# Performance work log

Measured on AMD Instinct MI355X. Metric: run time of the kernel, lower is better.

## Reference

```python
import jax, jax.numpy as jnp
import numpy as np

T, MEM, B, DM, N, D = 1024, 1024, 4, 1024, 16, 64
C = MEM + T
SCALE = 1.0 / D ** 0.5
LN_EPS = 1e-5


def _rel_shift(x):
    # x: [T, C, B, N] -> Transformer-XL relative shift
    t, c = x.shape[0], x.shape[1]
    zero_pad = jnp.zeros((t, 1) + x.shape[2:], x.dtype)
    x_padded = jnp.concatenate([zero_pad, x], axis=1)  # [T, C+1, B, N]
    x_padded = x_padded.reshape((c + 1, t) + x.shape[2:])
    return x_padded[1:].reshape(x.shape)


def setup_inputs() -> dict:
    key = jax.random.key(0)
    ks = jax.random.split(key, 8)
    h = jax.random.normal(ks[0], (T, B, DM), jnp.float32)
    m = jax.random.normal(ks[1], (MEM, B, DM), jnp.float32)
    r = jax.random.normal(ks[2], (C, DM), jnp.float32)
    # causal mask with memory: query i (global pos MEM+i) may attend to j <= MEM+i
    mask = (jnp.arange(C)[None, :] > (jnp.arange(T)[:, None] + MEM))[:, :, None]  # [T,C,1] bool, True=disallow
    W_qkv = jax.random.normal(ks[3], (DM, 3 * N * D), jnp.float32) * 0.02
    W_r = jax.random.normal(ks[4], (DM, N * D), jnp.float32) * 0.02
    W_o = jax.random.normal(ks[5], (N * D, DM), jnp.float32) * 0.02
    r_w_bias = jax.random.normal(ks[6], (N, D), jnp.float32)
    r_r_bias = jax.random.normal(ks[7], (N, D), jnp.float32)
    ln_gamma = jnp.ones((DM,), jnp.float32)
    ln_beta = jnp.zeros((DM,), jnp.float32)
    return {"h": h, "m": m, "r": r, "mask": mask, "W_qkv": W_qkv, "W_r": W_r,
            "W_o": W_o, "r_w_bias": r_w_bias, "r_r_bias": r_r_bias,
            "ln_gamma": ln_gamma, "ln_beta": ln_beta}


def reference(h, m, r, mask, W_qkv, W_r, W_o, r_w_bias, r_r_bias, ln_gamma, ln_beta):
    t, b = h.shape[0], h.shape[1]
    c = r.shape[0]
    cat = jnp.concatenate([m, h], axis=0)          # [C, B, DM]
    w_heads = cat @ W_qkv                           # [C, B, 3*N*D]
    w_q, w_k, w_v = jnp.split(w_heads, 3, axis=-1)
    w_q = w_q[-t:].reshape(t, b, N, D)              # [T,B,N,D]
    w_k = w_k.reshape(c, b, N, D)                   # [C,B,N,D]
    w_v = w_v.reshape(c, b, N, D)                   # [C,B,N,D]
    r_k = (r @ W_r).reshape(c, N, D)                # [C,N,D]
    AC = jnp.einsum('ibnd,jbnd->ijbn', w_q + r_w_bias, w_k)
    BD = jnp.einsum('ibnd,jnd->ijbn', w_q + r_r_bias, r_k)
    BD = _rel_shift(BD)
    score = (AC + BD) * SCALE                       # [T,C,B,N]
    score = jnp.where(mask[:, :, :, None], jnp.float32(-65000.0), score.astype(jnp.float32)).astype(score.dtype)
    prob = jax.nn.softmax(score, axis=1)
    vec = jnp.einsum('ijbn,jbnd->ibnd', prob, w_v).reshape(t, b, N * D)
    attn_out = vec @ W_o                            # [T,B,DM]
    x = h + attn_out
    mu = jnp.mean(x, axis=-1, keepdims=True)
    var = jnp.mean((x - mu) ** 2, axis=-1, keepdims=True)
    return (x - mu) * jax.lax.rsqrt(var + LN_EPS) * ln_gamma + ln_beta
```

## Files before the change

### kernel.cpp

```cpp
#include <hip/hip_runtime.h>
#include <stdint.h>

#define T_LEN 1024
#define MEM_LEN 1024
#define C_LEN 2048
#define B_SZ 4
#define DM_ 1024
#define NH 16
#define HD 64

typedef __attribute__((ext_vector_type(8))) short short8;
typedef __attribute__((ext_vector_type(4))) float f32x4;
typedef __attribute__((ext_vector_type(4))) unsigned short ushort4v;
typedef __attribute__((ext_vector_type(8))) unsigned short ushort8v;
typedef __attribute__((ext_vector_type(4))) float float4v;

__device__ __forceinline__ unsigned short f2bf(float f) {
  union { float f; unsigned int u; } v; v.f = f;
  unsigned int r = v.u + 0x7fffu + ((v.u >> 16) & 1u);
  return (unsigned short)(r >> 16);
}
__device__ __forceinline__ float bf2f(unsigned short b) {
  union { unsigned int u; float f; } v; v.u = ((unsigned int)b) << 16;
  return v.f;
}
__device__ __forceinline__ unsigned int cvtpk(float lo, float hi) {
  unsigned int r;
  asm("v_cvt_pk_bf16_f32 %0, %1, %2" : "=v"(r) : "v"(lo), "v"(hi));
  return r;
}
__device__ __forceinline__ f32x4 mfma16(short8 a, short8 b, f32x4 c) {
  return __builtin_amdgcn_mfma_f32_16x16x32_bf16(a, b, c, 0, 0, 0);
}

__global__ void k_convert_all(const float* __restrict__ m, const float* __restrict__ h,
                              const float* __restrict__ r,
                              unsigned short* __restrict__ catB,
                              unsigned short* __restrict__ rB) {
  int idx = blockIdx.x * 256 + threadIdx.x;
  const int MQ = (MEM_LEN * B_SZ * DM_) / 4;
  const int CQ = 2 * MQ;
  float4v v;
  unsigned short* dst;
  int di;
  if (idx < MQ)      { v = ((const float4v*)m)[idx];       dst = catB; di = idx; }
  else if (idx < CQ) { v = ((const float4v*)h)[idx - MQ];  dst = catB; di = idx; }
  else               { v = ((const float4v*)r)[idx - CQ];  dst = rB;   di = idx - CQ; }
  ushort4v o;
  o.x = f2bf(v.x); o.y = f2bf(v.y); o.z = f2bf(v.z); o.w = f2bf(v.w);
  ((ushort4v*)dst)[di] = o;
}

__global__ void k_transpose_w(const float* __restrict__ Wqkv, const float* __restrict__ Wr,
                              const float* __restrict__ Wo,
                              unsigned short* __restrict__ WqkvT, unsigned short* __restrict__ WrT,
                              unsigned short* __restrict__ WoT) {
  __shared__ float tile[32][33];
  const int z = blockIdx.z;
  const int Ccols = (z == 0) ? 3072 : 1024;
  if (blockIdx.x * 32 >= Ccols) return;
  const float* in = (z == 0) ? Wqkv : (z == 1) ? Wr : Wo;
  unsigned short* out = (z == 0) ? WqkvT : (z == 1) ? WrT : WoT;
  int c0 = blockIdx.x * 32, r0 = blockIdx.y * 32;
  int tx = threadIdx.x & 31, ty = threadIdx.x >> 5;
#pragma unroll
  for (int p = 0; p < 4; ++p)
    tile[ty + 8 * p][tx] = in[(size_t)(r0 + ty + 8 * p) * Ccols + c0 + tx];
  __syncthreads();
#pragma unroll
  for (int p = 0; p < 4; ++p)
    out[(size_t)(c0 + ty + 8 * p) * 1024 + r0 + tx] = f2bf(tile[tx][ty + 8 * p]);
}

__global__ __launch_bounds__(256) void k_gemm_qkv(const unsigned short* __restrict__ catB,
                                                  const unsigned short* __restrict__ rB,
                                                  const unsigned short* __restrict__ WqkvT,
                                                  const unsigned short* __restrict__ WrT,
                                                  unsigned short* __restrict__ Kp,
                                                  unsigned short* __restrict__ Vp,
                                                  unsigned short* __restrict__ Qp,
                                                  unsigned short* __restrict__ Rkp) {
  __shared__ unsigned short As[128 * 64];
  __shared__ unsigned short Bs[128 * 64];
  const int tid = threadIdx.x;
  const int w = tid >> 6, l = tid & 63;
  const int wm = w >> 1, wn = w & 1;
  const int lg = l >> 4, lr = l & 15;
  const int bid = blockIdx.x;
  int mode, lpid, gx;
  const unsigned short *A, *BT;
  if (bid < 1024)      { mode = 2; lpid = bid;        gx = 16; A = catB;                        BT = WqkvT + (size_t)1024 * 1024; }
  else if (bid < 1280) { mode = 3; lpid = bid - 1024; gx = 8;  A = catB + (size_t)4096 * 1024;  BT = WqkvT; }
  else                 { mode = 4; lpid = bid - 1280; gx = 8;  A = rB;                          BT = WrT; }
  const int K = 1024;
  const int xcd = lpid & 7;
  const int idx = lpid >> 3;
  const int cb = idx % gx;
  const int rb = (idx / gx) * 8 + xcd;
  const int m0 = rb * 128, n0 = cb * 128;
  f32x4 acc[4][4] = {};
  const int lrow8 = l >> 3;
  const int scol = (l & 7) * 8;
  const unsigned short* Abase = A + (size_t)m0 * K;
  const unsigned short* Bbase = BT + (size_t)n0 * K;
  for (int kt = 0; kt < K; kt += 64) {
    __syncthreads();
#pragma unroll
    for (int q = 0; q < 4; ++q) {
      int chunk = w * 4 + q;
      int row = chunk * 8 + lrow8;
      __builtin_amdgcn_global_load_lds(
          (const __attribute__((address_space(1))) void*)(Abase + (size_t)row * K + kt + scol),
          (__attribute__((address_space(3))) void*)(As + chunk * 512), 16, 0, 0);
      __builtin_amdgcn_global_load_lds(
          (const __attribute__((address_space(1))) void*)(Bbase + (size_t)row * K + kt + scol),
          (__attribute__((address_space(3))) void*)(Bs + chunk * 512), 16, 0, 0);
    }
    __syncthreads();
#pragma unroll
    for (int ks = 0; ks < 2; ++ks) {
      short8 a[4], bb[4];
#pragma unroll
      for (int mi = 0; mi < 4; ++mi)
        a[mi] = *(const short8*)&As[(wm * 64 + mi * 16 + lr) * 64 + ks * 32 + lg * 8];
#pragma unroll
      for (int ni = 0; ni < 4; ++ni)
        bb[ni] = *(const short8*)&Bs[(wn * 64 + ni * 16 + lr) * 64 + ks * 32 + lg * 8];
#pragma unroll
      for (int mi = 0; mi < 4; ++mi)
#pragma unroll
        for (int ni = 0; ni < 4; ++ni)
          acc[mi][ni] = mfma16(a[mi], bb[ni], acc[mi][ni]);
    }
  }
#pragma unroll
  for (int mi = 0; mi < 4; ++mi)
#pragma unroll
    for (int ni = 0; ni < 4; ++ni)
#pragma unroll
      for (int r = 0; r < 4; ++r) {
        int row = m0 + wm * 64 + mi * 16 + lg * 4 + r;
        int cc = n0 + wn * 64 + ni * 16 + lr;
        float val = acc[mi][ni][r];
        if (mode == 2) {
          int nn = (cc & 1023) >> 6, d = cc & 63;
          int c = row >> 2, b = row & 3;
          size_t addr = ((size_t)((b * 16 + nn) * 2048 + c)) * 64 + d;
          unsigned short* dst = (cc < 1024) ? Kp : Vp;
          dst[addr] = f2bf(val);
        } else if (mode == 3) {
          int nn = cc >> 6, d = cc & 63;
          int t = row >> 2, b = row & 3;
          Qp[((size_t)((b * 16 + nn) * 1024 + t)) * 64 + d] = f2bf(val);
        } else {
          int nn = cc >> 6, d = cc & 63;
          Rkp[((size_t)(nn * 2048 + row)) * 64 + d] = f2bf(val);
        }
      }
}

__global__ __launch_bounds__(256) void k_gemm_o(const unsigned short* __restrict__ A,
                                                const unsigned short* __restrict__ BT,
                                                float* __restrict__ Cout, int M, int N, int K) {
  __shared__ unsigned short As[128 * 64];
  __shared__ unsigned short Bs[128 * 64];
  const int tid = threadIdx.x;
  const int w = tid >> 6, l = tid & 63;
  const int wm = w >> 1, wn = w & 1;
  const int lg = l >> 4, lr = l & 15;
  const int gx = gridDim.x;
  const int pid = blockIdx.y * gx + blockIdx.x;
  const int xcd = pid & 7;
  const int idx = pid >> 3;
  const int cb = idx % gx;
  const int rb = (idx / gx) * 8 + xcd;
  const int m0 = rb * 128, n0 = cb * 128;
  f32x4 acc[4][4] = {};
  const int lrow8 = l >> 3;
  const int scol = (l & 7) * 8;
  const unsigned short* Abase = A + (size_t)m0 * K;
  const unsigned short* Bbase = BT + (size_t)n0 * K;
  for (int kt = 0; kt < K; kt += 64) {
    __syncthreads();
#pragma unroll
    for (int q = 0; q < 4; ++q) {
      int chunk = w * 4 + q;
      int row = chunk * 8 + lrow8;
      __builtin_amdgcn_global_load_lds(
          (const __attribute__((address_space(1))) void*)(Abase + (size_t)row * K + kt + scol),
          (__attribute__((address_space(3))) void*)(As + chunk * 512), 16, 0, 0);
      __builtin_amdgcn_global_load_lds(
          (const __attribute__((address_space(1))) void*)(Bbase + (size_t)row * K + kt + scol),
          (__attribute__((address_space(3))) void*)(Bs + chunk * 512), 16, 0, 0);
    }
    __syncthreads();
#pragma unroll
    for (int ks = 0; ks < 2; ++ks) {
      short8 a[4], bb[4];
#pragma unroll
      for (int mi = 0; mi < 4; ++mi)
        a[mi] = *(const short8*)&As[(wm * 64 + mi * 16 + lr) * 64 + ks * 32 + lg * 8];
#pragma unroll
      for (int ni = 0; ni < 4; ++ni)
        bb[ni] = *(const short8*)&Bs[(wn * 64 + ni * 16 + lr) * 64 + ks * 32 + lg * 8];
#pragma unroll
      for (int mi = 0; mi < 4; ++mi)
#pragma unroll
        for (int ni = 0; ni < 4; ++ni)
          acc[mi][ni] = mfma16(a[mi], bb[ni], acc[mi][ni]);
    }
  }
#pragma unroll
  for (int mi = 0; mi < 4; ++mi)
#pragma unroll
    for (int ni = 0; ni < 4; ++ni)
#pragma unroll
      for (int r = 0; r < 4; ++r) {
        int row = m0 + wm * 64 + mi * 16 + lg * 4 + r;
        int cc = n0 + wn * 64 + ni * 16 + lr;
        Cout[(size_t)row * N + cc] = acc[mi][ni][r];
      }
}

__global__ void k_vt(const unsigned short* __restrict__ Vp, unsigned short* __restrict__ VT) {
  __shared__ unsigned short tile[64][72];
  int c0 = blockIdx.x * 64;
  int n = blockIdx.y, b = blockIdx.z;
  int t = threadIdx.x;
  const unsigned short* src = Vp + ((size_t)((b * 16 + n) * 2048 + c0)) * 64;
#pragma unroll
  for (int p = 0; p < 16; ++p) {
    int idx = p * 256 + t;
    int r = idx >> 6, d = idx & 63;
    tile[d][r] = src[(size_t)r * 64 + d];
  }
  __syncthreads();
#pragma unroll
  for (int p = 0; p < 16; ++p) {
    int idx = p * 256 + t;
    int d = idx >> 6, c = idx & 63;
    VT[(size_t)((b * 16 + n) * 64 + d) * 2048 + c0 + c] = tile[d][c];
  }
}

__device__ __forceinline__ void stage_tile(const unsigned short* __restrict__ Kbase,
                                           const unsigned short* __restrict__ Vbase,
                                           unsigned short* ksBuf, unsigned short* vsBuf,
                                           int j0, int tid) {
#pragma unroll
  for (int q = 0; q < 2; ++q) {
    int chunk = q * 256 + tid;
    int row = chunk >> 3;
    int slot = chunk & 7;
    int ss = slot ^ (row & 7);
    __builtin_amdgcn_global_load_lds(
        (const __attribute__((address_space(1))) void*)(Kbase + (size_t)(j0 + row) * 64 + ss * 8),
        (__attribute__((address_space(3))) void*)(ksBuf + chunk * 8), 16, 0, 0);
    __builtin_amdgcn_global_load_lds(
        (const __attribute__((address_space(1))) void*)(Vbase + (size_t)row * 2048 + j0 + ss * 8),
        (__attribute__((address_space(3))) void*)(vsBuf + chunk * 8), 16, 0, 0);
  }
}

__global__ __launch_bounds__(256) void k_attn(const unsigned short* __restrict__ Qp,
                                              const unsigned short* __restrict__ Kp,
                                              const unsigned short* __restrict__ VT,
                                              const unsigned short* __restrict__ Rkp,
                                              const float* __restrict__ rwb,
                                              const float* __restrict__ rrb,
                                              unsigned short* __restrict__ po,
                                              float* __restrict__ psumG) {
  __shared__ __align__(16) unsigned short Ks[2][64 * 64];
  __shared__ __align__(16) unsigned short Vs[2][64 * 64];
  __shared__ unsigned short P[4][16][72];
  const int tid = threadIdx.x;
  const int w = tid >> 6, l = tid & 63;
  const int lg = l >> 4, lr = l & 15;
  const int L = blockIdx.x;
  const int bnlo = L & 7;
  const int rest = L >> 3;
  const int bnhi = rest / 48;
  const int inner = rest - bnhi * 48;
  const int xt = inner / 3;
  const int s  = inner - xt * 3;
  const int bn = bnhi * 8 + bnlo;
  const int i0 = xt * 64;
  const int n = bn & 15, b = bn >> 4;
  const int wrow = i0 + w * 16;

  const int ntile = xt + 17;
  const int t0 = (s * ntile) / 3;
  const int t1 = ((s + 1) * ntile) / 3;

  const unsigned short* Kbase = Kp + (size_t)bn * 2048 * 64;
  const unsigned short* Vbase = VT + (size_t)bn * 64 * 2048;
  const unsigned short* Rkbase = Rkp + (size_t)n * 2048 * 64;

  short8 aq0u, aq1u, aq0v, aq1v;
  {
    const unsigned short* qp = Qp + (size_t)(bn * 1024 + wrow + lr) * 64 + lg * 8;
    short8 q0 = *(const short8*)qp;
    short8 q1 = *(const short8*)(qp + 32);
    const float* up = rwb + n * 64 + lg * 8;
    const float* vp = rrb + n * 64 + lg * 8;
#pragma unroll
    for (int e = 0; e < 8; ++e) {
      float q0f = bf2f((unsigned short)q0[e]);
      float q1f = bf2f((unsigned short)q1[e]);
      aq0u[e] = (short)f2bf(q0f + up[e]);
      aq1u[e] = (short)f2bf(q1f + up[e + 32]);
      aq0v[e] = (short)f2bf(q0f + vp[e]);
      aq1v[e] = (short)f2bf(q1f + vp[e + 32]);
    }
  }
  float psum[4];
  f32x4 o[4];
#pragma unroll
  for (int r = 0; r < 4; ++r) psum[r] = 0.f;
#pragma unroll
  for (int df = 0; df < 4; ++df) o[df] = (f32x4){0.f, 0.f, 0.f, 0.f};

  stage_tile(Kbase, Vbase, Ks[0], Vs[0], t0 * 64, tid);
  stage_tile(Kbase, Vbase, Ks[1], Vs[1], (t0 + 1) * 64, tid);

  const float EXPC = 0.18033688011112042f;

  for (int jt = t0; jt < t1; ++jt) {
    const int j0 = jt * 64;
    const int cur = (jt - t0) & 1;
    if (jt + 1 < t1) { asm volatile("s_waitcnt vmcnt(4)" ::: "memory"); }
    else             { asm volatile("s_waitcnt vmcnt(0)" ::: "memory"); }
    __builtin_amdgcn_s_barrier();

    f32x4 sac[4];
#pragma unroll
    for (int jf = 0; jf < 4; ++jf) sac[jf] = (f32x4){0.f, 0.f, 0.f, 0.f};
    __builtin_amdgcn_s_setprio(1);
#pragma unroll
    for (int jf = 0; jf < 4; ++jf) {
      int row = jf * 16 + lr;
      int rx = row & 7;
      short8 k0 = *(const short8*)&Ks[cur][row * 64 + ((lg ^ rx) * 8)];
      short8 k1 = *(const short8*)&Ks[cur][row * 64 + (((4 + lg) ^ rx) * 8)];
      sac[jf] = mfma16(aq0u, k0, sac[jf]);
      sac[jf] = mfma16(aq1u, k1, sac[jf]);
    }
    __builtin_amdgcn_s_setprio(0);
    const int kbw = j0 + 1008 - i0 - w * 16;
    f32x4 gb[5];
#pragma unroll
    for (int jg = 0; jg < 5; ++jg) {
      int rowK = kbw + jg * 16 + lr;
      short8 b0 = {}, b1 = {};
      if (rowK < C_LEN) {
        const unsigned short* rp = Rkbase + (size_t)rowK * 64 + lg * 8;
        b0 = *(const short8*)rp;
        b1 = *(const short8*)(rp + 32);
      }
      f32x4 g = (f32x4){0.f, 0.f, 0.f, 0.f};
      g = mfma16(aq0v, b0, g);
      g = mfma16(aq1v, b1, g);
      gb[jg] = g;
    }
    const bool needMask = (j0 + 63 > i0 + w * 16 + MEM_LEN);
    float p[4][4];
#pragma unroll
    for (int r = 0; r < 4; ++r) {
      const int R = lg * 4 + r;
      const int delta = lr + 15 - R;
      const int src = (l & 48) | (delta & 15);
      float v0 = __shfl(gb[0][r], src);
      float v1 = __shfl(gb[1][r], src);
      float v2 = __shfl(gb[2][r], src);
      float v3 = __shfl(gb[3][r], src);
      float v4 = __shfl(gb[4][r], src);
      const bool hi = delta >= 16;
      float bd0 = hi ? v1 : v0;
      float bd1 = hi ? v2 : v1;
      float bd2 = hi ? v3 : v2;
      float bd3 = hi ? v4 : v3;
      float e0 = exp2f((sac[0][r] + bd0) * EXPC);
      float e1 = exp2f((sac[1][r] + bd1) * EXPC);
      float e2 = exp2f((sac[2][r] + bd2) * EXPC);
      float e3 = exp2f((sac[3][r] + bd3) * EXPC);
      if (needMask) {
        const int jlim = i0 + w * 16 + R + MEM_LEN;
        int j = j0 + lr;
        e0 = (j > jlim) ? 0.f : e0;  j += 16;
        e1 = (j > jlim) ? 0.f : e1;  j += 16;
        e2 = (j > jlim) ? 0.f : e2;  j += 16;
        e3 = (j > jlim) ? 0.f : e3;
      }
      p[0][r] = e0; p[1][r] = e1; p[2][r] = e2; p[3][r] = e3;
    }
#pragma unroll
    for (int jf = 0; jf < 4; ++jf)
#pragma unroll
      for (int r = 0; r < 4; ++r) psum[r] += p[jf][r];
#pragma unroll
    for (int r = 0; r < 4; ++r) {
      unsigned int a01 = cvtpk(p[0][r], p[1][r]);
      unsigned int a23 = cvtpk(p[2][r], p[3][r]);
      const int R = lg * 4 + r;
      P[w][R][lr]      = (unsigned short)a01;
      P[w][R][16 + lr] = (unsigned short)(a01 >> 16);
      P[w][R][32 + lr] = (unsigned short)a23;
      P[w][R][48 + lr] = (unsigned short)(a23 >> 16);
    }
    __builtin_amdgcn_s_setprio(1);
#pragma unroll
    for (int ks = 0; ks < 2; ++ks) {
      short8 ap = *(const short8*)&P[w][lr][ks * 32 + lg * 8];
#pragma unroll
      for (int df = 0; df < 4; ++df) {
        int row = df * 16 + lr;
        int rx = row & 7;
        short8 vv = *(const short8*)&Vs[cur][row * 64 + (((ks * 4 + lg) ^ rx) * 8)];
        o[df] = mfma16(ap, vv, o[df]);
      }
    }
    __builtin_amdgcn_s_setprio(0);
    __builtin_amdgcn_s_barrier();
    if (jt + 2 < t1)
      stage_tile(Kbase, Vbase, Ks[cur], Vs[cur], (jt + 2) * 64, tid);
  }
  const int pbase = (bn * 16 + xt) * 3 + s;
  unsigned short* poB = po + (size_t)pbase * 4096;
#pragma unroll
  for (int r = 0; r < 4; ++r) {
    float v = psum[r];
    v += __shfl_xor(v, 1);
    v += __shfl_xor(v, 2);
    v += __shfl_xor(v, 4);
    v += __shfl_xor(v, 8);
    if (lr == 0) psumG[pbase * 64 + w * 16 + lg * 4 + r] = v;
  }
#pragma unroll
  for (int df = 0; df < 4; ++df)
#pragma unroll
    for (int r = 0; r < 4; ++r)
      poB[(w * 16 + lg * 4 + r) * 64 + df * 16 + lr] = f2bf(o[df][r]);
}

__global__ __launch_bounds__(256) void k_ared(const unsigned short* __restrict__ po,
                                              const float* __restrict__ psumG,
                                              unsigned short* __restrict__ vec) {
  const int idx = blockIdx.x;
  const int tid = threadIdx.x;
  const int bn = idx >> 4, xt = idx & 15;
  const int b = bn >> 4, n = bn & 15;
  __shared__ float rs[64];
  if (tid < 64) {
    const float* q = psumG + idx * 192;
    rs[tid] = q[tid] + q[tid + 64] + q[tid + 128];
  }
  __syncthreads();
  const ushort8v* p0 = (const ushort8v*)(po + (size_t)(idx * 3 + 0) * 4096);
  const ushort8v* p1 = (const ushort8v*)(po + (size_t)(idx * 3 + 1) * 4096);
  const ushort8v* p2 = (const ushort8v*)(po + (size_t)(idx * 3 + 2) * 4096);
#pragma unroll
  for (int k = 0; k < 2; ++k) {
    int e = tid + k * 256;
    int row = e >> 3, d8 = e & 7;
    ushort8v a = p0[e], bb = p1[e], c = p2[e];
    float inv = 1.f / rs[row];
    int t = xt * 64 + row;
    ushort8v ov;
#pragma unroll
    for (int q = 0; q < 8; ++q)
      ov[q] = f2bf((bf2f(a[q]) + bf2f(bb[q]) + bf2f(c[q])) * inv);
    *(ushort8v*)&vec[(size_t)(t * 4 + b) * 1024 + n * 64 + d8 * 8] = ov;
  }
}

__global__ __launch_bounds__(256) void k_ln(const float* __restrict__ xg, const float* __restrict__ h,
                                            const float* __restrict__ gamma, const float* __restrict__ beta,
                                            float* __restrict__ out) {
  const int row = blockIdx.x;
  const int t = threadIdx.x;
  __shared__ float red1[4], red2[4];
  float4v xv = ((const float4v*)(xg + (size_t)row * 1024))[t];
  float4v hv = ((const float4v*)(h + (size_t)row * 1024))[t];
  float x0 = xv.x + hv.x, x1 = xv.y + hv.y, x2 = xv.z + hv.z, x3 = xv.w + hv.w;
  float s = x0 + x1 + x2 + x3;
#pragma unroll
  for (int off = 1; off < 64; off <<= 1) s += __shfl_xor(s, off);
  if ((t & 63) == 0) red1[t >> 6] = s;
  __syncthreads();
  float mean = (red1[0] + red1[1] + red1[2] + red1[3]) * (1.f / 1024.f);
  float d0 = x0 - mean, d1 = x1 - mean, d2 = x2 - mean, d3 = x3 - mean;
  float q = d0 * d0 + d1 * d1 + d2 * d2 + d3 * d3;
#pragma unroll
  for (int off = 1; off < 64; off <<= 1) q += __shfl_xor(q, off);
  if ((t & 63) == 0) red2[t >> 6] = q;
  __syncthreads();
  float var = (red2[0] + red2[1] + red2[2] + red2[3]) * (1.f / 1024.f);
  float rs = rsqrtf(var + 1e-5f);
  float4v gv = ((const float4v*)gamma)[t];
  float4v bv = ((const float4v*)beta)[t];
  float4v ov;
  ov.x = d0 * rs * gv.x + bv.x;
  ov.y = d1 * rs * gv.y + bv.y;
  ov.z = d2 * rs * gv.z + bv.z;
  ov.w = d3 * rs * gv.w + bv.w;
  ((float4v*)(out + (size_t)row * 1024))[t] = ov;
}

extern "C" void kernel_launch(void* const* d_in, const int* in_sizes, int n_in,
                              void* d_out, int out_size, void* d_ws, size_t ws_size,
                              hipStream_t stream) {
  (void)in_sizes; (void)n_in; (void)out_size; (void)ws_size;
  const float* h    = (const float*)d_in[0];
  const float* m    = (const float*)d_in[1];
  const float* r    = (const float*)d_in[2];
  const float* Wqkv = (const float*)d_in[4];
  const float* Wr   = (const float*)d_in[5];
  const float* Wo   = (const float*)d_in[6];
  const float* rwb  = (const float*)d_in[7];
  const float* rrb  = (const float*)d_in[8];
  const float* gam  = (const float*)d_in[9];
  const float* bet  = (const float*)d_in[10];
  float* out = (float*)d_out;

  char* ws = (char*)d_ws;
  unsigned short* catB   = (unsigned short*)(ws + 0);
  unsigned short* WqkvT  = (unsigned short*)(ws + 16777216);
  unsigned short* WrT    = (unsigned short*)(ws + 23068672);
  unsigned short* WoT    = (unsigned short*)(ws + 25165824);
  unsigned short* Vp     = (unsigned short*)(ws + 27262976);
  unsigned short* po     = (unsigned short*)(ws + 44040192);
  unsigned short* VT     = (unsigned short*)(ws + 81788928);
  unsigned short* vec    = (unsigned short*)(ws + 99221504);
  float* xbuf            = (float*)(ws + 107610112);
  unsigned short* rB     = (unsigned short*)(ws + 124387328);
  unsigned short* Kp     = (unsigned short*)(ws + 128581632);
  unsigned short* Qp     = (unsigned short*)(ws + 145358848);
  unsigned short* Rkp    = (unsigned short*)(ws + 153747456);
  float* psumG = (float*)(ws + 124387328);

  hipLaunchKernelGGL(k_convert_all, dim3(10240), dim3(256), 0, stream, m, h, r, catB, rB);
  hipLaunchKernelGGL(k_transpose_w, dim3(96, 32, 3), dim3(256), 0, stream,
                     Wqkv, Wr, Wo, WqkvT, WrT, WoT);
  hipLaunchKernelGGL(k_gemm_qkv, dim3(1408), dim3(256), 0, stream,
                     catB, rB, WqkvT, WrT, Kp, Vp, Qp, Rkp);
  hipLaunchKernelGGL(k_vt, dim3(32, 16, 4), dim3(256), 0, stream, Vp, VT);
  hipLaunchKernelGGL(k_attn, dim3(3072), dim3(256), 0, stream, Qp, Kp, VT, Rkp, rwb, rrb, po, psumG);
  hipLaunchKernelGGL(k_ared, dim3(1024), dim3(256), 0, stream, po, psumG, vec);
  hipLaunchKernelGGL(k_gemm_o, dim3(8, 32), dim3(256), 0, stream, vec, WoT, xbuf, 4096, 1024, 1024);
  hipLaunchKernelGGL(k_ln, dim3(4096), dim3(256), 0, stream, xbuf, h, gam, bet, out);
}
```

Measured before the change: 307.4 us.

## Rewrite QKV projection GEMM as 256x256 tile, 8-wave, pipelined LDS kernel

```diff
diff --git a/kernel.cpp b/kernel.cpp
--- a/kernel.cpp
+++ b/kernel.cpp
@@ -72,75 +72,120 @@
     out[(size_t)(c0 + ty + 8 * p) * 1024 + r0 + tx] = f2bf(tile[tx][ty + 8 * p]);
 }
 
-__global__ __launch_bounds__(256) void k_gemm_qkv(const unsigned short* __restrict__ catB,
-                                                  const unsigned short* __restrict__ rB,
-                                                  const unsigned short* __restrict__ WqkvT,
-                                                  const unsigned short* __restrict__ WrT,
-                                                  unsigned short* __restrict__ Kp,
-                                                  unsigned short* __restrict__ Vp,
-                                                  unsigned short* __restrict__ Qp,
-                                                  unsigned short* __restrict__ Rkp) {
-  __shared__ unsigned short As[128 * 64];
-  __shared__ unsigned short Bs[128 * 64];
+__device__ __forceinline__ void stage_half_g(const unsigned short* __restrict__ src, int ldK,
+                                             unsigned short* dst, int tid) {
+#pragma unroll
+  for (int q = 0; q < 2; ++q) {
+    int idx = q * 512 + tid;
+    int row = idx >> 3;
+    int g = idx & 7;
+    int gs = g ^ (((row >> 2) & 1) << 1);
+    __builtin_amdgcn_global_load_lds(
+        (const __attribute__((address_space(1))) void*)(src + (size_t)row * ldK + gs * 8),
+        (__attribute__((address_space(3))) void*)(dst + idx * 8), 16, 0, 0);
+  }
+}
+__device__ __forceinline__ short8 frag_rd(const unsigned short* half, int row, int kg) {
+  int g = kg ^ (((row >> 2) & 1) << 1);
+  return *(const short8*)&half[row * 64 + g * 8];
+}
+
+__global__ __launch_bounds__(512, 2) void k_gemm_qkv8(const unsigned short* __restrict__ catB,
+                                                      const unsigned short* __restrict__ rB,
+                                                      const unsigned short* __restrict__ WqkvT,
+                                                      const unsigned short* __restrict__ WrT,
+                                                      unsigned short* __restrict__ Kp,
+                                                      unsigned short* __restrict__ Vp,
+                                                      unsigned short* __restrict__ Qp,
+                                                      unsigned short* __restrict__ Rkp) {
+  __shared__ unsigned short Ash[4][128 * 64];
+  __shared__ unsigned short Bsh[4][128 * 64];
   const int tid = threadIdx.x;
   const int w = tid >> 6, l = tid & 63;
-  const int wm = w >> 1, wn = w & 1;
+  const int wr = w >> 2, wc = w & 3;
   const int lg = l >> 4, lr = l & 15;
   const int bid = blockIdx.x;
   int mode, lpid, gx;
   const unsigned short *A, *BT;
-  if (bid < 1024)      { mode = 2; lpid = bid;        gx = 16; A = catB;                        BT = WqkvT + (size_t)1024 * 1024; }
-  else if (bid < 1280) { mode = 3; lpid = bid - 1024; gx = 8;  A = catB + (size_t)4096 * 1024;  BT = WqkvT; }
-  else                 { mode = 4; lpid = bid - 1280; gx = 8;  A = rB;                          BT = WrT; }
-  const int K = 1024;
+  if (bid < 256)      { mode = 2; lpid = bid;       gx = 8; A = catB;                      BT = WqkvT + (size_t)1024 * 1024; }
+  else if (bid < 320) { mode = 3; lpid = bid - 256; gx = 4; A = catB + (size_t)4096 * 1024; BT = WqkvT; }
+  else                { mode = 4; lpid = bid - 320; gx = 4; A = rB;                        BT = WrT; }
+  const int K = 1024, NT = 16;
   const int xcd = lpid & 7;
   const int idx = lpid >> 3;
   const int cb = idx % gx;
   const int rb = (idx / gx) * 8 + xcd;
-  const int m0 = rb * 128, n0 = cb * 128;
-  f32x4 acc[4][4] = {};
-  const int lrow8 = l >> 3;
-  const int scol = (l & 7) * 8;
-  const unsigned short* Abase = A + (size_t)m0 * K;
-  const unsigned short* Bbase = BT + (size_t)n0 * K;
-  for (int kt = 0; kt < K; kt += 64) {
-    __syncthreads();
-#pragma unroll
-    for (int q = 0; q < 4; ++q) {
-      int chunk = w * 4 + q;
-      int row = chunk * 8 + lrow8;
-      __builtin_amdgcn_global_load_lds(
-          (const __attribute__((address_space(1))) void*)(Abase + (size_t)row * K + kt + scol),
-          (__attribute__((address_space(3))) void*)(As + chunk * 512), 16, 0, 0);
-      __builtin_amdgcn_global_load_lds(
-          (const __attribute__((address_space(1))) void*)(Bbase + (size_t)row * K + kt + scol),
-          (__attribute__((address_space(3))) void*)(Bs + chunk * 512), 16, 0, 0);
-    }
-    __syncthreads();
-#pragma unroll
-    for (int ks = 0; ks < 2; ++ks) {
-      short8 a[4], bb[4];
-#pragma unroll
-      for (int mi = 0; mi < 4; ++mi)
-        a[mi] = *(const short8*)&As[(wm * 64 + mi * 16 + lr) * 64 + ks * 32 + lg * 8];
-#pragma unroll
-      for (int ni = 0; ni < 4; ++ni)
-        bb[ni] = *(const short8*)&Bs[(wn * 64 + ni * 16 + lr) * 64 + ks * 32 + lg * 8];
-#pragma unroll
-      for (int mi = 0; mi < 4; ++mi)
+  const int m0 = rb * 256, n0 = cb * 256;
+  const unsigned short* Ab = A + (size_t)m0 * K;
+  const unsigned short* Bb = BT + (size_t)n0 * K;
+
+  f32x4 acc[8][4];
+#pragma unroll
+  for (int i = 0; i < 8; ++i)
+#pragma unroll
+    for (int j = 0; j < 4; ++j) acc[i][j] = (f32x4){0.f, 0.f, 0.f, 0.f};
+
+  stage_half_g(Bb,                       K, Bsh[0], tid);
+  stage_half_g(Bb + (size_t)128 * K,     K, Bsh[1], tid);
+  stage_half_g(Ab,                       K, Ash[0], tid);
+  stage_half_g(Ab + (size_t)128 * K,     K, Ash[1], tid);
+  asm volatile("s_waitcnt vmcnt(4)" ::: "memory");
+  stage_half_g(Bb + 64,                   K, Bsh[2], tid);
+  stage_half_g(Bb + (size_t)128 * K + 64, K, Bsh[3], tid);
+  stage_half_g(Ab + 64,                   K, Ash[2], tid);
+  asm volatile("s_waitcnt vmcnt(6)" ::: "memory");
+  __builtin_amdgcn_s_barrier();
+
+  for (int t = 0; t < NT; ++t) {
+    const unsigned short* Ah = Ash[(2 * t + wr) & 3];
+    const unsigned short* Bh = Bsh[(2 * t + (wc >> 1)) & 3];
+    const int brow = (wc & 1) * 64;
+    short8 bf[4][2];
+#pragma unroll
+    for (int p = 0; p < 4; ++p) {
+      if (p == 0) {
 #pragma unroll
         for (int ni = 0; ni < 4; ++ni)
-          acc[mi][ni] = mfma16(a[mi], bb[ni], acc[mi][ni]);
-    }
-  }
-#pragma unroll
-  for (int mi = 0; mi < 4; ++mi)
+#pragma unroll
+          for (int ks = 0; ks < 2; ++ks)
+            bf[ni][ks] = frag_rd(Bh, brow + ni * 16 + lr, ks * 4 + lg);
+      }
+      short8 af[2][2];
+#pragma unroll
+      for (int j = 0; j < 2; ++j)
+#pragma unroll
+        for (int ks = 0; ks < 2; ++ks)
+          af[j][ks] = frag_rd(Ah, (2 * p + j) * 16 + lr, ks * 4 + lg);
+      if (p == 0)      { if (t + 1 < NT) stage_half_g(Ab + (size_t)128 * K + (t + 1) * 64, K, Ash[(2 * t + 3) & 3], tid); }
+      else if (p == 1) { if (t + 2 < NT) stage_half_g(Bb + (t + 2) * 64,                   K, Bsh[(2 * t + 4) & 3], tid); }
+      else if (p == 2) { if (t + 2 < NT) stage_half_g(Bb + (size_t)128 * K + (t + 2) * 64, K, Bsh[(2 * t + 5) & 3], tid); }
+      else             { if (t + 2 < NT) stage_half_g(Ab + (t + 2) * 64,                   K, Ash[(2 * t + 4) & 3], tid); }
+      __builtin_amdgcn_s_barrier();
+      asm volatile("s_waitcnt lgkmcnt(0)" ::: "memory");
+      __builtin_amdgcn_s_setprio(1);
+#pragma unroll
+      for (int j = 0; j < 2; ++j)
+#pragma unroll
+        for (int ni = 0; ni < 4; ++ni)
+#pragma unroll
+          for (int ks = 0; ks < 2; ++ks)
+            acc[2 * p + j][ni] = mfma16(af[j][ks], bf[ni][ks], acc[2 * p + j][ni]);
+      __builtin_amdgcn_s_setprio(0);
+      if (p == 3) {
+        if (t < NT - 2)       { asm volatile("s_waitcnt vmcnt(6)" ::: "memory"); }
+        else if (t == NT - 2) { asm volatile("s_waitcnt vmcnt(0)" ::: "memory"); }
+      }
+      __builtin_amdgcn_s_barrier();
+    }
+  }
+#pragma unroll
+  for (int mi = 0; mi < 8; ++mi)
 #pragma unroll
     for (int ni = 0; ni < 4; ++ni)
 #pragma unroll
       for (int r = 0; r < 4; ++r) {
-        int row = m0 + wm * 64 + mi * 16 + lg * 4 + r;
-        int cc = n0 + wn * 64 + ni * 16 + lr;
+        int row = m0 + wr * 128 + mi * 16 + lg * 4 + r;
+        int cc = n0 + wc * 64 + ni * 16 + lr;
         float val = acc[mi][ni][r];
         if (mode == 2) {
           int nn = (cc & 1023) >> 6, d = cc & 63;
@@ -150,8 +195,8 @@
           dst[addr] = f2bf(val);
         } else if (mode == 3) {
           int nn = cc >> 6, d = cc & 63;
-          int t = row >> 2, b = row & 3;
-          Qp[((size_t)((b * 16 + nn) * 1024 + t)) * 64 + d] = f2bf(val);
+          int t2 = row >> 2, b = row & 3;
+          Qp[((size_t)((b * 16 + nn) * 1024 + t2)) * 64 + d] = f2bf(val);
         } else {
           int nn = cc >> 6, d = cc & 63;
           Rkp[((size_t)(nn * 2048 + row)) * 64 + d] = f2bf(val);
@@ -541,7 +586,7 @@
   hipLaunchKernelGGL(k_convert_all, dim3(10240), dim3(256), 0, stream, m, h, r, catB, rB);
   hipLaunchKernelGGL(k_transpose_w, dim3(96, 32, 3), dim3(256), 0, stream,
                      Wqkv, Wr, Wo, WqkvT, WrT, WoT);
-  hipLaunchKernelGGL(k_gemm_qkv, dim3(1408), dim3(256), 0, stream,
+  hipLaunchKernelGGL(k_gemm_qkv8, dim3(352), dim3(512), 0, stream,
                      catB, rB, WqkvT, WrT, Kp, Vp, Qp, Rkp);
   hipLaunchKernelGGL(k_vt, dim3(32, 16, 4), dim3(256), 0, stream, Vp, VT);
   hipLaunchKernelGGL(k_attn, dim3(3072), dim3(256), 0, stream, Qp, Kp, VT, Rkp, rwb, rrb, po, psumG);
```

Measured after the change: 305.3 us. About the same (-0.7%).
